# Optimization experiments

Measured on AMD Instinct MI355X. Metric: run time of the kernel, lower is better.

Reference implementation:

```python
import jax, jax.numpy as jnp
import numpy as np

B, N, D = 4, 4096, 256
DENSITY = 0.02


def setup_inputs() -> dict:
    key = jax.random.key(0)
    kx, ka1, ka2, kwt, kbt, kwh, kth = jax.random.split(key, 7)
    x = jax.random.normal(kx, (B, N, D), dtype=jnp.float32)
    # sparse weighted adjacency, materialized densely for the reference
    mask = jax.random.uniform(ka1, (B, N, N)) < DENSITY
    vals = jax.random.uniform(ka2, (B, N, N), dtype=jnp.float32)
    adj = jnp.where(mask, vals, 0.0).astype(jnp.float32)
    s = 0.02  # random_normal initializer stddev
    W_t = s * jax.random.normal(kwt, (D, D), dtype=jnp.float32)
    b_t = s * jax.random.normal(kbt, (D,), dtype=jnp.float32)
    W_h = s * jax.random.normal(kwh, (D, D), dtype=jnp.float32)
    theta = s * jax.random.normal(kth, (D, D), dtype=jnp.float32)
    return {"x": x, "adj": adj, "W_t": W_t, "b_t": b_t, "W_h": W_h, "theta": theta}


def reference(x, adj, W_t, b_t, W_h, theta):
    # degree normalization: norm = (deg + 1e-6)^{-1/2}
    in_degrees = jnp.sum(adj, axis=-1)                      # [B, N]
    norm = jnp.power(in_degrees + 1e-6, -0.5)[..., None]    # [B, N, 1]
    # homophilic path: D^{-1/2} A D^{-1/2} (x theta)
    f_hom = jnp.einsum('bnd,de->bne', x, theta) * norm      # [B, N, D]
    f_hom = jnp.einsum('bnm,bmd->bnd', adj, f_hom) * norm   # batched SpMM (dense ref)
    # heterophilic path
    f_het = jnp.einsum('bnd,de->bne', x, W_h)
    # gate and fuse
    gate = jax.nn.sigmoid(jnp.einsum('bnd,de->bne', x, W_t) + b_t)
    out = gate * f_hom + (1.0 - gate) * f_het
    return jax.nn.elu(out)
```

## Files before the change

### kernel.cpp

```cpp
#include <hip/hip_runtime.h>
#include <math.h>

constexpr int Bn = 4;
constexpr int Nn = 4096;
constexpr int Dd = 256;
constexpr int Mrows = Bn * Nn;
constexpr int CAP = 192;

typedef __attribute__((ext_vector_type(8))) short short8;
typedef __attribute__((ext_vector_type(4))) float f32x4;

__device__ __forceinline__ unsigned short f2bf(float f) {
    unsigned int u = __float_as_uint(f);
    u = (u + 0x7FFFu + ((u >> 16) & 1u)) >> 16;
    return (unsigned short)u;
}

__global__ __launch_bounds__(256) void prep_kernel(
    const float* __restrict__ x, const float* __restrict__ theta,
    const float* __restrict__ Wh, const float* __restrict__ Wt,
    unsigned short* __restrict__ xb, unsigned short* __restrict__ WT) {
    const int tid = threadIdx.x;
    if (blockIdx.x < 4096) {
        const size_t idx = (size_t)blockIdx.x * 1024 + tid * 4;
        float4 v = *(const float4*)(x + idx);
        ushort4 o;
        o.x = f2bf(v.x); o.y = f2bf(v.y); o.z = f2bf(v.z); o.w = f2bf(v.w);
        *(ushort4*)(xb + idx) = o;
    } else {
        const int b2 = blockIdx.x - 4096;
        const int m = b2 >> 8;
        const int c = b2 & 255;
        const float* src = (m == 0) ? theta : (m == 1 ? Wh : Wt);
        WT[(size_t)m * 65536 + (size_t)c * 256 + tid] = f2bf(src[(size_t)tid * 256 + c]);
    }
}

__global__ __launch_bounds__(256) void build_csr_kernel(
    const float* __restrict__ adj, float* __restrict__ norm,
    int* __restrict__ cntg, int* __restrict__ csr_idx, float* __restrict__ csr_val) {
    const int row = blockIdx.x;
    const int tid = threadIdx.x;
    __shared__ int lcnt;
    __shared__ int ml[CAP];
    __shared__ float vl[CAP];
    __shared__ float wsum[4];
    if (tid == 0) lcnt = 0;
    __syncthreads();

    const float* arow = adj + (size_t)row * Nn;
    float s = 0.f;
#pragma unroll
    for (int seg = 0; seg < 4; ++seg) {
        const int base = seg * 1024 + tid * 4;
        float4 v = *(const float4*)(arow + base);
        s += v.x + v.y + v.z + v.w;
        float vv[4] = {v.x, v.y, v.z, v.w};
#pragma unroll
        for (int j = 0; j < 4; ++j) {
            if (vv[j] != 0.f) {
                int p = atomicAdd(&lcnt, 1);
                if (p < CAP) { ml[p] = base + j; vl[p] = vv[j]; }
            }
        }
    }
#pragma unroll
    for (int off = 32; off; off >>= 1) s += __shfl_down(s, off, 64);
    if ((tid & 63) == 0) wsum[tid >> 6] = s;
    __syncthreads();

    const int cc = min(lcnt, CAP);
    if (tid == 0) {
        float d = wsum[0] + wsum[1] + wsum[2] + wsum[3];
        norm[row] = 1.0f / sqrtf(d + 1e-6f);
        cntg[row] = cc;
    }
    if (tid < cc) {
        csr_idx[(size_t)row * CAP + tid] = ml[tid];
        csr_val[(size_t)row * CAP + tid] = vl[tid];
    }
}

__global__ __launch_bounds__(256) void gemm_kernel(
    const unsigned short* __restrict__ xb, const unsigned short* __restrict__ WT,
    const float* __restrict__ bt, const float* __restrict__ norm,
    float* __restrict__ T, float* __restrict__ H, float* __restrict__ G) {
    __shared__ unsigned short As[128][40];
    __shared__ unsigned short Bs[128][40];

    const int tid = threadIdx.x;
    const int l = tid & 63;
    const int w = tid >> 6;
    const int wr = w >> 1, wc = w & 1;
    const int l15 = l & 15, l4 = l >> 4;
    const int rowbase = blockIdx.x * 128;
    const int my = blockIdx.y >> 1;
    const int cb = (blockIdx.y & 1) * 128;
    const unsigned short* wm = WT + (size_t)my * 65536;

    f32x4 acc[4][4];
#pragma unroll
    for (int m = 0; m < 4; ++m)
#pragma unroll
        for (int n = 0; n < 4; ++n) acc[m][n] = (f32x4)0.f;

    for (int k0 = 0; k0 < 256; k0 += 32) {
#pragma unroll
        for (int i = 0; i < 2; ++i) {
            const int c = tid + 256 * i;
            const int r = c >> 2, ko = (c & 3) * 8;
            *(int4*)&As[r][ko] = *(const int4*)(xb + (size_t)(rowbase + r) * 256 + k0 + ko);
            *(int4*)&Bs[r][ko] = *(const int4*)(wm + (size_t)(cb + r) * 256 + k0 + ko);
        }
        __syncthreads();
        short8 af[4], bf[4];
#pragma unroll
        for (int m = 0; m < 4; ++m) af[m] = *(short8*)&As[wr * 64 + m * 16 + l15][l4 * 8];
#pragma unroll
        for (int n = 0; n < 4; ++n) bf[n] = *(short8*)&Bs[wc * 64 + n * 16 + l15][l4 * 8];
#pragma unroll
        for (int m = 0; m < 4; ++m)
#pragma unroll
            for (int n = 0; n < 4; ++n)
                acc[m][n] = __builtin_amdgcn_mfma_f32_16x16x32_bf16(af[m], bf[n], acc[m][n], 0, 0, 0);
        __syncthreads();
    }

#pragma unroll
    for (int m = 0; m < 4; ++m) {
#pragma unroll
        for (int n = 0; n < 4; ++n) {
            const int col = cb + wc * 64 + n * 16 + l15;
#pragma unroll
            for (int j = 0; j < 4; ++j) {
                const int gr = rowbase + wr * 64 + m * 16 + l4 * 4 + j;
                const size_t o = (size_t)gr * 256 + col;
                const float v = acc[m][n][j];
                if (my == 0) {
                    T[o] = v * norm[gr];
                } else if (my == 1) {
                    H[o] = v;
                } else {
                    G[o] = 1.f / (1.f + expf(-(v + bt[col])));
                }
            }
        }
    }
}

__global__ __launch_bounds__(256) void spmm_fuse_kernel(
    const int* __restrict__ cntg, const int* __restrict__ csr_idx,
    const float* __restrict__ csr_val, const float* __restrict__ T,
    const float* __restrict__ H, const float* __restrict__ G,
    const float* __restrict__ norm, float* __restrict__ out) {
    const int row = blockIdx.x;
    const int b = row >> 12;
    const int tid = threadIdx.x;

    __shared__ int ml[CAP];
    __shared__ float vl[CAP];

    const int c = cntg[row];
    if (tid < c) {
        ml[tid] = csr_idx[(size_t)row * CAP + tid];
        vl[tid] = csr_val[(size_t)row * CAP + tid];
    }
    __syncthreads();

    const float* tb = T + (size_t)b * Nn * Dd;
    float acc = 0.f;
    int i = 0;
    for (; i + 4 <= c; i += 4) {
        int m0 = ml[i], m1 = ml[i + 1], m2 = ml[i + 2], m3 = ml[i + 3];
        float w0 = vl[i], w1 = vl[i + 1], w2 = vl[i + 2], w3 = vl[i + 3];
        float t0 = tb[(size_t)m0 * Dd + tid];
        float t1 = tb[(size_t)m1 * Dd + tid];
        float t2 = tb[(size_t)m2 * Dd + tid];
        float t3 = tb[(size_t)m3 * Dd + tid];
        acc = fmaf(w0, t0, acc);
        acc = fmaf(w1, t1, acc);
        acc = fmaf(w2, t2, acc);
        acc = fmaf(w3, t3, acc);
    }
    for (; i < c; ++i) acc = fmaf(vl[i], tb[(size_t)ml[i] * Dd + tid], acc);

    const float fh = acc * norm[row];
    const size_t o = (size_t)row * Dd + tid;
    const float g = G[o];
    const float h = H[o];
    float val = g * fh + (1.f - g) * h;
    out[o] = val > 0.f ? val : expf(val) - 1.f;
}

extern "C" void kernel_launch(void* const* d_in, const int* in_sizes, int n_in,
                              void* d_out, int out_size, void* d_ws, size_t ws_size,
                              hipStream_t stream) {
    const float* x     = (const float*)d_in[0];
    const float* adj   = (const float*)d_in[1];
    const float* W_t   = (const float*)d_in[2];
    const float* b_t   = (const float*)d_in[3];
    const float* W_h   = (const float*)d_in[4];
    const float* theta = (const float*)d_in[5];
    float* out = (float*)d_out;

    char* p = (char*)d_ws;
    float* norm   = (float*)p;                 p += (size_t)Mrows * 4;
    int*   cntg   = (int*)p;                   p += (size_t)Mrows * 4;
    int*   csridx = (int*)p;                   p += (size_t)Mrows * CAP * 4;
    float* csrval = (float*)p;                 p += (size_t)Mrows * CAP * 4;
    unsigned short* xb = (unsigned short*)p;   p += (size_t)Mrows * Dd * 2;
    unsigned short* WT = (unsigned short*)p;   p += (size_t)3 * 256 * 256 * 2;
    float* T = (float*)p;                      p += (size_t)Mrows * Dd * 4;
    float* H = (float*)p;                      p += (size_t)Mrows * Dd * 4;
    float* G = (float*)p;

    prep_kernel<<<4096 + 768, 256, 0, stream>>>(x, theta, W_h, W_t, xb, WT);
    build_csr_kernel<<<Mrows, 256, 0, stream>>>(adj, norm, cntg, csridx, csrval);
    dim3 gg(128, 6);
    gemm_kernel<<<gg, 256, 0, stream>>>(xb, WT, b_t, norm, T, H, G);
    spmm_fuse_kernel<<<Mrows, 256, 0, stream>>>(cntg, csridx, csrval, T, H, G, norm, out);
}
```

Baseline: 479.6 us.

## Merge GEMM and CSR build into one launch, store T and edges in bf16

Combines the projection GEMM and adjacency CSR-build kernels into a single launch with block-index branching, so the compute-bound GEMM blocks can overlap the bandwidth-bound adjacency scan. The column normalization moves into the SpMM edge weights, which lets T be stored as bf16. Edge index and value are packed into one 32-bit word. The SpMM gathers bf16 rows with eight independent accumulators and remaps block IDs so rows from the same batch share an XCD's cache. The cost is extra bf16 rounding of T and of the edge values, which adds precision error, plus a larger mixed grid.

Result: slower. 491.1 us (+2.4%).

```diff
diff --git a/kernel.cpp b/kernel.cpp
--- a/kernel.cpp
+++ b/kernel.cpp
@@ -1,11 +1,11 @@
 #include <hip/hip_runtime.h>
 #include <math.h>
 
-constexpr int Bn = 4;
 constexpr int Nn = 4096;
 constexpr int Dd = 256;
-constexpr int Mrows = Bn * Nn;
+constexpr int Mrows = 16384;
 constexpr int CAP = 192;
+constexpr int GEMM_BLOCKS = 768;
 
 typedef __attribute__((ext_vector_type(8))) short short8;
 typedef __attribute__((ext_vector_type(4))) float f32x4;
@@ -14,6 +14,9 @@
     unsigned int u = __float_as_uint(f);
     u = (u + 0x7FFFu + ((u >> 16) & 1u)) >> 16;
     return (unsigned short)u;
+}
+__device__ __forceinline__ float bf2f(unsigned short u) {
+    return __uint_as_float((unsigned int)u << 16);
 }
 
 __global__ __launch_bounds__(256) void prep_kernel(
@@ -36,159 +39,165 @@
     }
 }
 
-__global__ __launch_bounds__(256) void build_csr_kernel(
-    const float* __restrict__ adj, float* __restrict__ norm,
-    int* __restrict__ cntg, int* __restrict__ csr_idx, float* __restrict__ csr_val) {
-    const int row = blockIdx.x;
+__global__ __launch_bounds__(256) void fused_kernel(
+    const float* __restrict__ adj,
+    const unsigned short* __restrict__ xb, const unsigned short* __restrict__ WT,
+    const float* __restrict__ bt,
+    float* __restrict__ norm, int* __restrict__ cntg, unsigned int* __restrict__ edges,
+    unsigned short* __restrict__ T, float* __restrict__ H, float* __restrict__ G) {
+    __shared__ __align__(16) char smraw[2 * 128 * 40 * 2];
     const int tid = threadIdx.x;
-    __shared__ int lcnt;
-    __shared__ int ml[CAP];
-    __shared__ float vl[CAP];
-    __shared__ float wsum[4];
-    if (tid == 0) lcnt = 0;
-    __syncthreads();
-
-    const float* arow = adj + (size_t)row * Nn;
-    float s = 0.f;
-#pragma unroll
-    for (int seg = 0; seg < 4; ++seg) {
-        const int base = seg * 1024 + tid * 4;
-        float4 v = *(const float4*)(arow + base);
-        s += v.x + v.y + v.z + v.w;
-        float vv[4] = {v.x, v.y, v.z, v.w};
-#pragma unroll
-        for (int j = 0; j < 4; ++j) {
-            if (vv[j] != 0.f) {
-                int p = atomicAdd(&lcnt, 1);
-                if (p < CAP) { ml[p] = base + j; vl[p] = vv[j]; }
+
+    if (blockIdx.x < GEMM_BLOCKS) {
+        auto As = (unsigned short(*)[40])smraw;
+        auto Bs = (unsigned short(*)[40])(smraw + 128 * 40 * 2);
+        const int bid = blockIdx.x;
+        const int rowbase = (bid & 127) * 128;
+        const int y = bid >> 7;
+        const int my = y >> 1;
+        const int cb = (y & 1) * 128;
+        const unsigned short* wm = WT + (size_t)my * 65536;
+
+        const int l = tid & 63;
+        const int w = tid >> 6;
+        const int wr = w >> 1, wc = w & 1;
+        const int l15 = l & 15, l4 = l >> 4;
+
+        f32x4 acc[4][4];
+#pragma unroll
+        for (int m = 0; m < 4; ++m)
+#pragma unroll
+            for (int n = 0; n < 4; ++n) acc[m][n] = (f32x4)0.f;
+
+        for (int k0 = 0; k0 < 256; k0 += 32) {
+#pragma unroll
+            for (int i = 0; i < 2; ++i) {
+                const int c = tid + 256 * i;
+                const int r = c >> 2, ko = (c & 3) * 8;
+                *(int4*)&As[r][ko] = *(const int4*)(xb + (size_t)(rowbase + r) * 256 + k0 + ko);
+                *(int4*)&Bs[r][ko] = *(const int4*)(wm + (size_t)(cb + r) * 256 + k0 + ko);
             }
-        }
-    }
-#pragma unroll
-    for (int off = 32; off; off >>= 1) s += __shfl_down(s, off, 64);
-    if ((tid & 63) == 0) wsum[tid >> 6] = s;
-    __syncthreads();
-
-    const int cc = min(lcnt, CAP);
-    if (tid == 0) {
-        float d = wsum[0] + wsum[1] + wsum[2] + wsum[3];
-        norm[row] = 1.0f / sqrtf(d + 1e-6f);
-        cntg[row] = cc;
-    }
-    if (tid < cc) {
-        csr_idx[(size_t)row * CAP + tid] = ml[tid];
-        csr_val[(size_t)row * CAP + tid] = vl[tid];
-    }
-}
-
-__global__ __launch_bounds__(256) void gemm_kernel(
-    const unsigned short* __restrict__ xb, const unsigned short* __restrict__ WT,
-    const float* __restrict__ bt, const float* __restrict__ norm,
-    float* __restrict__ T, float* __restrict__ H, float* __restrict__ G) {
-    __shared__ unsigned short As[128][40];
-    __shared__ unsigned short Bs[128][40];
-
-    const int tid = threadIdx.x;
-    const int l = tid & 63;
-    const int w = tid >> 6;
-    const int wr = w >> 1, wc = w & 1;
-    const int l15 = l & 15, l4 = l >> 4;
-    const int rowbase = blockIdx.x * 128;
-    const int my = blockIdx.y >> 1;
-    const int cb = (blockIdx.y & 1) * 128;
-    const unsigned short* wm = WT + (size_t)my * 65536;
-
-    f32x4 acc[4][4];
-#pragma unroll
-    for (int m = 0; m < 4; ++m)
-#pragma unroll
-        for (int n = 0; n < 4; ++n) acc[m][n] = (f32x4)0.f;
-
-    for (int k0 = 0; k0 < 256; k0 += 32) {
-#pragma unroll
-        for (int i = 0; i < 2; ++i) {
-            const int c = tid + 256 * i;
-            const int r = c >> 2, ko = (c & 3) * 8;
-            *(int4*)&As[r][ko] = *(const int4*)(xb + (size_t)(rowbase + r) * 256 + k0 + ko);
-            *(int4*)&Bs[r][ko] = *(const int4*)(wm + (size_t)(cb + r) * 256 + k0 + ko);
-        }
-        __syncthreads();
-        short8 af[4], bf[4];
-#pragma unroll
-        for (int m = 0; m < 4; ++m) af[m] = *(short8*)&As[wr * 64 + m * 16 + l15][l4 * 8];
-#pragma unroll
-        for (int n = 0; n < 4; ++n) bf[n] = *(short8*)&Bs[wc * 64 + n * 16 + l15][l4 * 8];
-#pragma unroll
-        for (int m = 0; m < 4; ++m)
-#pragma unroll
-            for (int n = 0; n < 4; ++n)
-                acc[m][n] = __builtin_amdgcn_mfma_f32_16x16x32_bf16(af[m], bf[n], acc[m][n], 0, 0, 0);
-        __syncthreads();
-    }
-
-#pragma unroll
-    for (int m = 0; m < 4; ++m) {
-#pragma unroll
-        for (int n = 0; n < 4; ++n) {
-            const int col = cb + wc * 64 + n * 16 + l15;
-#pragma unroll
-            for (int j = 0; j < 4; ++j) {
-                const int gr = rowbase + wr * 64 + m * 16 + l4 * 4 + j;
-                const size_t o = (size_t)gr * 256 + col;
-                const float v = acc[m][n][j];
-                if (my == 0) {
-                    T[o] = v * norm[gr];
-                } else if (my == 1) {
-                    H[o] = v;
-                } else {
-                    G[o] = 1.f / (1.f + expf(-(v + bt[col])));
+            __syncthreads();
+            short8 af[4], bf[4];
+#pragma unroll
+            for (int m = 0; m < 4; ++m) af[m] = *(short8*)&As[wr * 64 + m * 16 + l15][l4 * 8];
+#pragma unroll
+            for (int n = 0; n < 4; ++n) bf[n] = *(short8*)&Bs[wc * 64 + n * 16 + l15][l4 * 8];
+#pragma unroll
+            for (int m = 0; m < 4; ++m)
+#pragma unroll
+                for (int n = 0; n < 4; ++n)
+                    acc[m][n] = __builtin_amdgcn_mfma_f32_16x16x32_bf16(af[m], bf[n], acc[m][n], 0, 0, 0);
+            __syncthreads();
+        }
+
+#pragma unroll
+        for (int m = 0; m < 4; ++m) {
+#pragma unroll
+            for (int n = 0; n < 4; ++n) {
+                const int col = cb + wc * 64 + n * 16 + l15;
+#pragma unroll
+                for (int j = 0; j < 4; ++j) {
+                    const int gr = rowbase + wr * 64 + m * 16 + l4 * 4 + j;
+                    const size_t o = (size_t)gr * 256 + col;
+                    const float v = acc[m][n][j];
+                    if (my == 0) {
+                        T[o] = f2bf(v);
+                    } else if (my == 1) {
+                        H[o] = v;
+                    } else {
+                        G[o] = 1.f / (1.f + expf(-(v + bt[col])));
+                    }
                 }
             }
         }
+    } else {
+        int* ml = (int*)smraw;
+        float* vl = (float*)(smraw + CAP * 4);
+        float* wsum = (float*)(smraw + CAP * 8);
+        int* lcnt = (int*)(smraw + CAP * 8 + 16);
+        const int row = blockIdx.x - GEMM_BLOCKS;
+        if (tid == 0) *lcnt = 0;
+        __syncthreads();
+
+        const float* arow = adj + (size_t)row * Nn;
+        float s = 0.f;
+#pragma unroll
+        for (int seg = 0; seg < 4; ++seg) {
+            const int base = seg * 1024 + tid * 4;
+            float4 v = *(const float4*)(arow + base);
+            s += v.x + v.y + v.z + v.w;
+            float vv[4] = {v.x, v.y, v.z, v.w};
+#pragma unroll
+            for (int j = 0; j < 4; ++j) {
+                if (vv[j] != 0.f) {
+                    int p = atomicAdd(lcnt, 1);
+                    if (p < CAP) { ml[p] = base + j; vl[p] = vv[j]; }
+                }
+            }
+        }
+#pragma unroll
+        for (int off = 32; off; off >>= 1) s += __shfl_down(s, off, 64);
+        if ((tid & 63) == 0) wsum[tid >> 6] = s;
+        __syncthreads();
+
+        const int cc = min(*lcnt, CAP);
+        if (tid == 0) {
+            float d = wsum[0] + wsum[1] + wsum[2] + wsum[3];
+            norm[row] = 1.0f / sqrtf(d + 1e-6f);
+            cntg[row] = cc;
+        }
+        if (tid < cc) {
+            edges[(size_t)row * CAP + tid] =
+                ((unsigned int)ml[tid] << 16) | (unsigned int)f2bf(vl[tid]);
+        }
     }
 }
 
 __global__ __launch_bounds__(256) void spmm_fuse_kernel(
-    const int* __restrict__ cntg, const int* __restrict__ csr_idx,
-    const float* __restrict__ csr_val, const float* __restrict__ T,
-    const float* __restrict__ H, const float* __restrict__ G,
-    const float* __restrict__ norm, float* __restrict__ out) {
-    const int row = blockIdx.x;
-    const int b = row >> 12;
+    const int* __restrict__ cntg, const unsigned int* __restrict__ edges,
+    const unsigned short* __restrict__ T, const float* __restrict__ H,
+    const float* __restrict__ G, const float* __restrict__ norm,
+    float* __restrict__ out) {
+    const int bid = blockIdx.x;
+    const int xcd = bid & 7;
+    const int b = xcd >> 1;
+    const int row = b * Nn + (xcd & 1) * 2048 + (bid >> 3);
     const int tid = threadIdx.x;
 
-    __shared__ int ml[CAP];
-    __shared__ float vl[CAP];
+    __shared__ int sml[CAP];
+    __shared__ float svl[CAP];
 
     const int c = cntg[row];
     if (tid < c) {
-        ml[tid] = csr_idx[(size_t)row * CAP + tid];
-        vl[tid] = csr_val[(size_t)row * CAP + tid];
+        const unsigned int pk = edges[(size_t)row * CAP + tid];
+        const int m = (int)(pk >> 16);
+        sml[tid] = m;
+        svl[tid] = bf2f((unsigned short)(pk & 0xFFFFu)) * norm[b * Nn + m];
     }
     __syncthreads();
 
-    const float* tb = T + (size_t)b * Nn * Dd;
-    float acc = 0.f;
+    const unsigned short* tb = T + (size_t)b * Nn * Dd;
+    float a0 = 0.f, a1 = 0.f, a2 = 0.f, a3 = 0.f, a4 = 0.f, a5 = 0.f, a6 = 0.f, a7 = 0.f;
     int i = 0;
-    for (; i + 4 <= c; i += 4) {
-        int m0 = ml[i], m1 = ml[i + 1], m2 = ml[i + 2], m3 = ml[i + 3];
-        float w0 = vl[i], w1 = vl[i + 1], w2 = vl[i + 2], w3 = vl[i + 3];
-        float t0 = tb[(size_t)m0 * Dd + tid];
-        float t1 = tb[(size_t)m1 * Dd + tid];
-        float t2 = tb[(size_t)m2 * Dd + tid];
-        float t3 = tb[(size_t)m3 * Dd + tid];
-        acc = fmaf(w0, t0, acc);
-        acc = fmaf(w1, t1, acc);
-        acc = fmaf(w2, t2, acc);
-        acc = fmaf(w3, t3, acc);
-    }
-    for (; i < c; ++i) acc = fmaf(vl[i], tb[(size_t)ml[i] * Dd + tid], acc);
+    for (; i + 8 <= c; i += 8) {
+        a0 = fmaf(svl[i + 0], bf2f(tb[(size_t)sml[i + 0] * Dd + tid]), a0);
+        a1 = fmaf(svl[i + 1], bf2f(tb[(size_t)sml[i + 1] * Dd + tid]), a1);
+        a2 = fmaf(svl[i + 2], bf2f(tb[(size_t)sml[i + 2] * Dd + tid]), a2);
+        a3 = fmaf(svl[i + 3], bf2f(tb[(size_t)sml[i + 3] * Dd + tid]), a3);
+        a4 = fmaf(svl[i + 4], bf2f(tb[(size_t)sml[i + 4] * Dd + tid]), a4);
+        a5 = fmaf(svl[i + 5], bf2f(tb[(size_t)sml[i + 5] * Dd + tid]), a5);
+        a6 = fmaf(svl[i + 6], bf2f(tb[(size_t)sml[i + 6] * Dd + tid]), a6);
+        a7 = fmaf(svl[i + 7], bf2f(tb[(size_t)sml[i + 7] * Dd + tid]), a7);
+    }
+    for (; i < c; ++i) a0 = fmaf(svl[i], bf2f(tb[(size_t)sml[i] * Dd + tid]), a0);
+    const float acc = ((a0 + a1) + (a2 + a3)) + ((a4 + a5) + (a6 + a7));
 
     const float fh = acc * norm[row];
     const size_t o = (size_t)row * Dd + tid;
     const float g = G[o];
     const float h = H[o];
-    float val = g * fh + (1.f - g) * h;
+    const float val = g * fh + (1.f - g) * h;
     out[o] = val > 0.f ? val : expf(val) - 1.f;
 }
 
@@ -206,17 +215,15 @@
     char* p = (char*)d_ws;
     float* norm   = (float*)p;                 p += (size_t)Mrows * 4;
     int*   cntg   = (int*)p;                   p += (size_t)Mrows * 4;
-    int*   csridx = (int*)p;                   p += (size_t)Mrows * CAP * 4;
-    float* csrval = (float*)p;                 p += (size_t)Mrows * CAP * 4;
+    unsigned int* edges = (unsigned int*)p;    p += (size_t)Mrows * CAP * 4;
     unsigned short* xb = (unsigned short*)p;   p += (size_t)Mrows * Dd * 2;
     unsigned short* WT = (unsigned short*)p;   p += (size_t)3 * 256 * 256 * 2;
-    float* T = (float*)p;                      p += (size_t)Mrows * Dd * 4;
+    unsigned short* T  = (unsigned short*)p;   p += (size_t)Mrows * Dd * 2;
     float* H = (float*)p;                      p += (size_t)Mrows * Dd * 4;
     float* G = (float*)p;
 
     prep_kernel<<<4096 + 768, 256, 0, stream>>>(x, theta, W_h, W_t, xb, WT);
-    build_csr_kernel<<<Mrows, 256, 0, stream>>>(adj, norm, cntg, csridx, csrval);
-    dim3 gg(128, 6);
-    gemm_kernel<<<gg, 256, 0, stream>>>(xb, WT, b_t, norm, T, H, G);
-    spmm_fuse_kernel<<<Mrows, 256, 0, stream>>>(cntg, csridx, csrval, T, H, G, norm, out);
-}
+    fused_kernel<<<GEMM_BLOCKS + Mrows, 256, 0, stream>>>(adj, xb, WT, b_t, norm, cntg,
+                                                          edges, T, H, G);
+    spmm_fuse_kernel<<<Mrows, 256, 0, stream>>>(cntg, edges, T, H, G, norm, out);
+}
```
